# Optimization experiments

Measured on AMD Instinct MI355X. Metric: run time of the kernel, lower is better.

Reference implementation:

```python
import jax, jax.numpy as jnp
import numpy as np

B, S, H = 32, 256, 128
K, C, DSUB, O = 8, 4096, 16, 6  # PQ subspaces, ncentroids=4096, subvector dim, bits/symbol


def setup_inputs() -> dict:
    key = jax.random.key(0)
    ks = jax.random.split(key, 8)
    return {
        "z": jax.random.normal(ks[0], (B, S, 3), jnp.float32),
        "W1": jax.random.normal(ks[1], (3, H), jnp.float32) * 0.3,
        "b1": jax.random.normal(ks[2], (H,), jnp.float32) * 0.1,
        "W2": jax.random.normal(ks[3], (H, H), jnp.float32) * 0.1,
        "b2": jax.random.normal(ks[4], (H,), jnp.float32) * 0.1,
        "centroids": jax.random.normal(ks[5], (K, C, DSUB), jnp.float32),
        "W3": jax.random.normal(ks[6], (H, O), jnp.float32) * 0.1,
        "b3": jax.random.normal(ks[7], (O,), jnp.float32) * 0.1,
    }


def reference(z, W1, b1, W2, b2, centroids, W3, b3):
    # Small demapper MLP (layers 1-2, exact dense math)
    h1 = jax.nn.relu(z @ W1 + b1)            # [B,S,H]
    h2 = jax.nn.relu(h1 @ W2 + b2)           # [B,S,H] == layer3in
    N = B * S
    x = h2.reshape(N, K, DSUB)               # split rows into K PQ subvectors
    # Encode: nearest centroid per subspace (||x-c||^2 argmin; ||x||^2 is constant per row)
    dots = jnp.einsum("nkd,kcd->nkc", x, centroids)      # [N,K,C]
    c_norm = jnp.sum(centroids * centroids, axis=-1)      # [K,C]
    codes = jnp.argmin(c_norm[None, :, :] - 2.0 * dots, axis=-1)  # [N,K] int
    # LUT: precomputed centroid @ W3 per subspace
    W3r = W3.reshape(K, DSUB, O)
    lut = jnp.einsum("kcd,kdo->kco", centroids, W3r)      # [K,C,O]
    # Approximate matmul: sum of LUT entries selected by codes
    approx = jnp.sum(lut[jnp.arange(K)[None, :], codes], axis=1)  # [N,O]
    llr = (approx + b3).reshape(B, S * O)                 # [B, n]
    return llr
```

## Files before the change

kernel.cpp:

```cpp
#include <hip/hip_runtime.h>
#include <stdint.h>

#define NROWS 8192
#define HDIM  128
#define KSUB  8
#define NC    4096
#define DSUB  16
#define OUTD  6

#define FB_TAU 4e-3f
#define DOTSCALE (-2.0f / 4096.0f)

typedef _Float16 f16x8 __attribute__((ext_vector_type(8)));
typedef float    f32x4 __attribute__((ext_vector_type(4)));

#define XK_OFF 0u
#define CN_OFF 4194304u
#define B1_OFF 4325376u
#define B2_OFF 6422528u
#define CO_OFF 8519680u
#define MG_OFF 8781824u

__global__ __launch_bounds__(256) void bprep_kernel(
    const float* __restrict__ ce, f16x8* __restrict__ B1, f16x8* __restrict__ B2)
{
    const int e = blockIdx.x * 256 + threadIdx.x;
    const int k    = e >> 14;
    const int tile = (e >> 6) & 255;
    const int lane = e & 63;
    const int col  = lane & 15;
    const int quad = lane >> 4;
    const int dims = (quad & 1) * 8;
    const int part = quad >> 1;
    const int n = tile * 16 + col;
    const float* cp = &ce[((size_t)k * NC + n) * DSUB + dims];
    f16x8 hi, lo;
    #pragma unroll
    for (int j = 0; j < 8; ++j) {
        const float s = cp[j] * 16.0f;
        const _Float16 h = (_Float16)s;
        hi[j] = h;
        lo[j] = (_Float16)(s - (float)h);
    }
    B1[e] = part ? lo : hi;
    B2[e] = part ? hi : lo;
}

__global__ __launch_bounds__(256) void mlp_kernel(
    const float* __restrict__ z, const float* __restrict__ W1, const float* __restrict__ b1,
    const float* __restrict__ W2, const float* __restrict__ b2,
    const float* __restrict__ centroids,
    float* __restrict__ xk, float* __restrict__ cnorm)
{
    __shared__ float h1s[32 * HDIM];
    __shared__ float w2s[HDIM * HDIM];
    const int t = threadIdx.x;
    const int row0 = blockIdx.x * 32;

    if (blockIdx.x < (KSUB * NC) / 256) {
        const int g = blockIdx.x * 256 + t;
        const float4* cp = (const float4*)&centroids[(size_t)g * DSUB];
        float nn = 0.f;
        #pragma unroll
        for (int q = 0; q < 4; ++q) {
            const float4 v = cp[q];
            nn = fmaf(v.x, v.x, nn); nn = fmaf(v.y, v.y, nn);
            nn = fmaf(v.z, v.z, nn); nn = fmaf(v.w, v.w, nn);
        }
        cnorm[g] = nn;
    }

    {
        const float4* g4 = (const float4*)W2;
        float4* s4 = (float4*)w2s;
        #pragma unroll
        for (int q = 0; q < 16; ++q) s4[t + q * 256] = g4[t + q * 256];
    }

    #pragma unroll
    for (int e = 0; e < 16; ++e) {
        const int idx = e * 256 + t;
        const int r = idx >> 7, j = idx & 127;
        const int n = row0 + r;
        float acc = b1[j];
        acc = fmaf(z[n * 3 + 0], W1[0 * HDIM + j], acc);
        acc = fmaf(z[n * 3 + 1], W1[1 * HDIM + j], acc);
        acc = fmaf(z[n * 3 + 2], W1[2 * HDIM + j], acc);
        h1s[idx] = fmaxf(acc, 0.f);
    }
    __syncthreads();

    const int c4 = (t & 31) * 4;
    const int r4 = (t >> 5) * 4;
    float acc[4][4];
    #pragma unroll
    for (int a = 0; a < 4; ++a)
        #pragma unroll
        for (int b = 0; b < 4; ++b) acc[a][b] = 0.f;

    for (int k4 = 0; k4 < HDIM; k4 += 4) {
        float hh[4][4], ww[4][4];
        #pragma unroll
        for (int q = 0; q < 4; ++q) {
            const float4 v = *(const float4*)&h1s[(r4 + q) * HDIM + k4];
            hh[q][0] = v.x; hh[q][1] = v.y; hh[q][2] = v.z; hh[q][3] = v.w;
        }
        #pragma unroll
        for (int p = 0; p < 4; ++p) {
            const float4 v = *(const float4*)&w2s[(k4 + p) * HDIM + c4];
            ww[p][0] = v.x; ww[p][1] = v.y; ww[p][2] = v.z; ww[p][3] = v.w;
        }
        #pragma unroll
        for (int q = 0; q < 4; ++q)
            #pragma unroll
            for (int p = 0; p < 4; ++p) {
                acc[q][0] = fmaf(hh[q][p], ww[p][0], acc[q][0]);
                acc[q][1] = fmaf(hh[q][p], ww[p][1], acc[q][1]);
                acc[q][2] = fmaf(hh[q][p], ww[p][2], acc[q][2]);
                acc[q][3] = fmaf(hh[q][p], ww[p][3], acc[q][3]);
            }
    }

    const float4 bb = *(const float4*)&b2[c4];
    const int kk = c4 >> 4;
    const int dd = c4 & 15;
    #pragma unroll
    for (int q = 0; q < 4; ++q) {
        float4 o;
        o.x = fmaxf(acc[q][0] + bb.x, 0.f);
        o.y = fmaxf(acc[q][1] + bb.y, 0.f);
        o.z = fmaxf(acc[q][2] + bb.z, 0.f);
        o.w = fmaxf(acc[q][3] + bb.w, 0.f);
        *(float4*)&xk[((size_t)kk * NROWS + (row0 + r4 + q)) * DSUB + dd] = o;
    }
}

__global__ __launch_bounds__(256) void argmin_kernel(
    const float* __restrict__ xk, const f16x8* __restrict__ B1,
    const f16x8* __restrict__ B2, const float* __restrict__ cnorm,
    int* __restrict__ codes, float* __restrict__ margin)
{
    const int t = threadIdx.x;
    const int lane = t & 63;
    const int wid  = t >> 6;
    const int bx = blockIdx.x;
    const int k  = bx >> 6;
    const int rb = (bx & 63) * 4 + wid;
    const int col  = lane & 15;
    const int quad = lane >> 4;
    const int dims = (quad & 1) * 8;
    const int part = quad >> 1;

    f16x8 A[2];
    #pragma unroll
    for (int g = 0; g < 2; ++g) {
        const int row = rb * 32 + g * 16 + col;
        const float* xp = &xk[((size_t)k * NROWS + row) * DSUB + dims];
        f16x8 hi, lo;
        #pragma unroll
        for (int j = 0; j < 8; ++j) {
            const float s = xp[j] * 256.0f;
            const _Float16 h = (_Float16)s;
            hi[j] = h;
            lo[j] = (_Float16)(s - (float)h);
        }
        A[g] = part ? lo : hi;
    }

    float m1[2][4], m2[2][4];
    int   idx[2][4];
    #pragma unroll
    for (int g = 0; g < 2; ++g)
        #pragma unroll
        for (int j = 0; j < 4; ++j) { m1[g][j] = 1e30f; m2[g][j] = 1e30f; idx[g][j] = 0; }

    const f16x8* b1p = &B1[((size_t)k * 256) * 64 + lane];
    const f16x8* b2p = &B2[((size_t)k * 256) * 64 + lane];
    const float* cnp = &cnorm[k * NC + col];

    #pragma unroll 2
    for (int tt = 0; tt < 256; ++tt) {
        const f16x8 b1 = b1p[tt * 64];
        const f16x8 b2 = b2p[tt * 64];
        const float nrm = cnp[tt * 16];
        f32x4 acc0 = {0.f, 0.f, 0.f, 0.f};
        f32x4 acc1 = {0.f, 0.f, 0.f, 0.f};
        acc0 = __builtin_amdgcn_mfma_f32_16x16x32_f16(A[0], b1, acc0, 0, 0, 0);
        acc0 = __builtin_amdgcn_mfma_f32_16x16x32_f16(A[0], b2, acc0, 0, 0, 0);
        acc1 = __builtin_amdgcn_mfma_f32_16x16x32_f16(A[1], b1, acc1, 0, 0, 0);
        acc1 = __builtin_amdgcn_mfma_f32_16x16x32_f16(A[1], b2, acc1, 0, 0, 0);
        const int c = tt * 16 + col;
        #pragma unroll
        for (int j = 0; j < 4; ++j) {
            {
                const float s = fmaf(acc0[j], DOTSCALE, nrm);
                const bool lt = s < m1[0][j];
                m2[0][j] = fminf(m2[0][j], fmaxf(m1[0][j], s));
                idx[0][j] = lt ? c : idx[0][j];
                m1[0][j] = fminf(s, m1[0][j]);
            }
            {
                const float s = fmaf(acc1[j], DOTSCALE, nrm);
                const bool lt = s < m1[1][j];
                m2[1][j] = fminf(m2[1][j], fmaxf(m1[1][j], s));
                idx[1][j] = lt ? c : idx[1][j];
                m1[1][j] = fminf(s, m1[1][j]);
            }
        }
    }

    #pragma unroll
    for (int off = 1; off < 16; off <<= 1) {
        #pragma unroll
        for (int g = 0; g < 2; ++g)
            #pragma unroll
            for (int j = 0; j < 4; ++j) {
                const float om1 = __shfl_xor(m1[g][j], off, 64);
                const float om2 = __shfl_xor(m2[g][j], off, 64);
                const int  oidx = __shfl_xor(idx[g][j], off, 64);
                const bool better = (om1 < m1[g][j]) ||
                                    (om1 == m1[g][j] && oidx < idx[g][j]);
                m2[g][j] = fminf(fminf(m2[g][j], om2), fmaxf(m1[g][j], om1));
                m1[g][j] = better ? om1 : m1[g][j];
                idx[g][j] = better ? oidx : idx[g][j];
            }
    }

    if (col == 0) {
        #pragma unroll
        for (int g = 0; g < 2; ++g)
            #pragma unroll
            for (int j = 0; j < 4; ++j) {
                const int row = rb * 32 + g * 16 + quad * 4 + j;
                codes[row * KSUB + k] = idx[g][j];
                margin[row * KSUB + k] = m2[g][j] - m1[g][j];
            }
    }
}

__global__ __launch_bounds__(256) void fallback_kernel(
    const float* __restrict__ xk, const float* __restrict__ ce,
    const float* __restrict__ cnorm, const float* __restrict__ margin,
    int* __restrict__ codes)
{
    const int wg = blockIdx.x * 4 + (threadIdx.x >> 6);
    const int lane = threadIdx.x & 63;
    if (margin[wg] >= FB_TAU) return;
    const int row = wg >> 3, k = wg & 7;

    float xr[DSUB];
    {
        const float* xp = &xk[((size_t)k * NROWS + row) * DSUB];
        #pragma unroll
        for (int q = 0; q < DSUB; q += 4) {
            const float4 v = *(const float4*)&xp[q];
            xr[q + 0] = -2.f * v.x; xr[q + 1] = -2.f * v.y;
            xr[q + 2] = -2.f * v.z; xr[q + 3] = -2.f * v.w;
        }
    }
    float m1 = 1e30f; int mi = NC;
    for (int c = lane; c < NC; c += 64) {
        const float* cp = &ce[((size_t)k * NC + c) * DSUB];
        float s = cnorm[k * NC + c];
        #pragma unroll
        for (int d = 0; d < DSUB; ++d) s = fmaf(xr[d], cp[d], s);
        if (s < m1) { m1 = s; mi = c; }
    }
    #pragma unroll
    for (int off = 1; off < 64; off <<= 1) {
        const float om1 = __shfl_xor(m1, off, 64);
        const int  omi = __shfl_xor(mi, off, 64);
        const bool better = (om1 < m1) || (om1 == m1 && omi < mi);
        m1 = better ? om1 : m1;
        mi = better ? omi : mi;
    }
    if (lane == 0) codes[wg] = mi;
}

__global__ __launch_bounds__(256) void out_kernel(
    const float* __restrict__ centroids, const float* __restrict__ W3,
    const float* __restrict__ b3, const int* __restrict__ codes,
    float* __restrict__ out)
{
    const int gid = blockIdx.x * 256 + threadIdx.x;
    const int n = gid / OUTD;
    const int o = gid - n * OUTD;
    float acc = b3[o];
    #pragma unroll
    for (int k = 0; k < KSUB; ++k) {
        const int code = codes[n * KSUB + k];
        const float* cp = &centroids[((size_t)k * NC + code) * DSUB];
        const float* wp = &W3[(k * DSUB) * OUTD + o];
        #pragma unroll
        for (int d = 0; d < DSUB; ++d)
            acc = fmaf(cp[d], wp[d * OUTD], acc);
    }
    out[gid] = acc;
}

extern "C" void kernel_launch(void* const* d_in, const int* in_sizes, int n_in,
                              void* d_out, int out_size, void* d_ws, size_t ws_size,
                              hipStream_t stream)
{
    const float* z  = (const float*)d_in[0];
    const float* W1 = (const float*)d_in[1];
    const float* b1 = (const float*)d_in[2];
    const float* W2 = (const float*)d_in[3];
    const float* b2 = (const float*)d_in[4];
    const float* ce = (const float*)d_in[5];
    const float* W3 = (const float*)d_in[6];
    const float* b3 = (const float*)d_in[7];

    char* ws = (char*)d_ws;
    float* xk     = (float*)(ws + XK_OFF);
    float* cnorm  = (float*)(ws + CN_OFF);
    f16x8* B1     = (f16x8*)(ws + B1_OFF);
    f16x8* B2     = (f16x8*)(ws + B2_OFF);
    int*   codes  = (int*)  (ws + CO_OFF);
    float* margin = (float*)(ws + MG_OFF);

    hipLaunchKernelGGL(bprep_kernel, dim3(512), dim3(256), 0, stream, ce, B1, B2);
    hipLaunchKernelGGL(mlp_kernel, dim3(NROWS / 32), dim3(256), 0, stream,
                       z, W1, b1, W2, b2, ce, xk, cnorm);
    hipLaunchKernelGGL(argmin_kernel, dim3(512), dim3(256), 0, stream,
                       xk, B1, B2, cnorm, codes, margin);
    hipLaunchKernelGGL(fallback_kernel, dim3(NROWS * KSUB / 4), dim3(256), 0, stream,
                       xk, ce, cnorm, margin, codes);
    hipLaunchKernelGGL(out_kernel, dim3((NROWS * OUTD) / 256), dim3(256), 0, stream,
                       ce, W3, b3, codes, (float*)d_out);
}
```

Before: 208.6 us.

## Split argmin centroid range across two blocks and merge partial minima in fallback

The argmin kernel now splits the 4096 centroids into two halves along grid z, doubling the block count. Each half writes a packed orderable (score, index) key plus its second-best score, and the fallback kernel merges the two halves before its margin test. The kernel also drops the separate B2 buffer by reading B1 with lane^32, software-prefetches the next tile, uses independent MFMAs instead of chained accumulation, and uses fmed3 for the second-min update. In exchange it adds workspace traffic and an extra merge step, and codes now aliases the B1 region.

Result: faster. 194.7 us (-6.6%).

```diff
diff --git a/kernel.cpp b/kernel.cpp
--- a/kernel.cpp
+++ b/kernel.cpp
@@ -17,12 +17,12 @@
 #define XK_OFF 0u
 #define CN_OFF 4194304u
 #define B1_OFF 4325376u
-#define B2_OFF 6422528u
-#define CO_OFF 8519680u
-#define MG_OFF 8781824u
+#define PK_OFF 6422528u
+#define M2_OFF 7471104u
+#define CO_OFF B1_OFF
 
 __global__ __launch_bounds__(256) void bprep_kernel(
-    const float* __restrict__ ce, f16x8* __restrict__ B1, f16x8* __restrict__ B2)
+    const float* __restrict__ ce, f16x8* __restrict__ B1)
 {
     const int e = blockIdx.x * 256 + threadIdx.x;
     const int k    = e >> 14;
@@ -43,7 +43,6 @@
         lo[j] = (_Float16)(s - (float)h);
     }
     B1[e] = part ? lo : hi;
-    B2[e] = part ? hi : lo;
 }
 
 __global__ __launch_bounds__(256) void mlp_kernel(
@@ -135,21 +134,22 @@
     }
 }
 
-__global__ __launch_bounds__(256) void argmin_kernel(
+__global__ __launch_bounds__(256, 4) void argmin_kernel(
     const float* __restrict__ xk, const f16x8* __restrict__ B1,
-    const f16x8* __restrict__ B2, const float* __restrict__ cnorm,
-    int* __restrict__ codes, float* __restrict__ margin)
+    const float* __restrict__ cnorm,
+    unsigned long long* __restrict__ pk, float* __restrict__ m2s)
 {
     const int t = threadIdx.x;
     const int lane = t & 63;
     const int wid  = t >> 6;
-    const int bx = blockIdx.x;
-    const int k  = bx >> 6;
-    const int rb = (bx & 63) * 4 + wid;
+    const int k  = blockIdx.y;
+    const int cz = blockIdx.z;
+    const int rb = blockIdx.x * 4 + wid;
     const int col  = lane & 15;
     const int quad = lane >> 4;
     const int dims = (quad & 1) * 8;
     const int part = quad >> 1;
+    const int ct0 = cz * 128;
 
     f16x8 A[2];
     #pragma unroll
@@ -174,35 +174,40 @@
         #pragma unroll
         for (int j = 0; j < 4; ++j) { m1[g][j] = 1e30f; m2[g][j] = 1e30f; idx[g][j] = 0; }
 
-    const f16x8* b1p = &B1[((size_t)k * 256) * 64 + lane];
-    const f16x8* b2p = &B2[((size_t)k * 256) * 64 + lane];
-    const float* cnp = &cnorm[k * NC + col];
-
-    #pragma unroll 2
-    for (int tt = 0; tt < 256; ++tt) {
-        const f16x8 b1 = b1p[tt * 64];
-        const f16x8 b2 = b2p[tt * 64];
-        const float nrm = cnp[tt * 16];
-        f32x4 acc0 = {0.f, 0.f, 0.f, 0.f};
-        f32x4 acc1 = {0.f, 0.f, 0.f, 0.f};
-        acc0 = __builtin_amdgcn_mfma_f32_16x16x32_f16(A[0], b1, acc0, 0, 0, 0);
-        acc0 = __builtin_amdgcn_mfma_f32_16x16x32_f16(A[0], b2, acc0, 0, 0, 0);
-        acc1 = __builtin_amdgcn_mfma_f32_16x16x32_f16(A[1], b1, acc1, 0, 0, 0);
-        acc1 = __builtin_amdgcn_mfma_f32_16x16x32_f16(A[1], b2, acc1, 0, 0, 0);
-        const int c = tt * 16 + col;
+    const f16x8* bp = &B1[((size_t)k * 256 + ct0) * 64];
+    const float* cnp = &cnorm[k * NC + ct0 * 16 + col];
+    const int l2 = lane ^ 32;
+
+    f16x8 cb1 = bp[lane], cb2 = bp[l2];
+    float cnv = cnp[0];
+
+    for (int tt = 0; tt < 128; ++tt) {
+        const f16x8 b1 = cb1, b2 = cb2;
+        const float nrm = cnv;
+        if (tt + 1 < 128) {
+            cb1 = bp[(tt + 1) * 64 + lane];
+            cb2 = bp[(tt + 1) * 64 + l2];
+            cnv = cnp[(tt + 1) * 16];
+        }
+        f32x4 z4 = {0.f, 0.f, 0.f, 0.f};
+        f32x4 a0a = __builtin_amdgcn_mfma_f32_16x16x32_f16(A[0], b1, z4, 0, 0, 0);
+        f32x4 a0b = __builtin_amdgcn_mfma_f32_16x16x32_f16(A[0], b2, z4, 0, 0, 0);
+        f32x4 a1a = __builtin_amdgcn_mfma_f32_16x16x32_f16(A[1], b1, z4, 0, 0, 0);
+        f32x4 a1b = __builtin_amdgcn_mfma_f32_16x16x32_f16(A[1], b2, z4, 0, 0, 0);
+        const int c = (ct0 + tt) * 16 + col;
         #pragma unroll
         for (int j = 0; j < 4; ++j) {
             {
-                const float s = fmaf(acc0[j], DOTSCALE, nrm);
+                const float s = fmaf(a0a[j] + a0b[j], DOTSCALE, nrm);
                 const bool lt = s < m1[0][j];
-                m2[0][j] = fminf(m2[0][j], fmaxf(m1[0][j], s));
+                m2[0][j] = __builtin_amdgcn_fmed3f(s, m1[0][j], m2[0][j]);
                 idx[0][j] = lt ? c : idx[0][j];
                 m1[0][j] = fminf(s, m1[0][j]);
             }
             {
-                const float s = fmaf(acc1[j], DOTSCALE, nrm);
+                const float s = fmaf(a1a[j] + a1b[j], DOTSCALE, nrm);
                 const bool lt = s < m1[1][j];
-                m2[1][j] = fminf(m2[1][j], fmaxf(m1[1][j], s));
+                m2[1][j] = __builtin_amdgcn_fmed3f(s, m1[1][j], m2[1][j]);
                 idx[1][j] = lt ? c : idx[1][j];
                 m1[1][j] = fminf(s, m1[1][j]);
             }
@@ -232,22 +237,38 @@
             #pragma unroll
             for (int j = 0; j < 4; ++j) {
                 const int row = rb * 32 + g * 16 + quad * 4 + j;
-                codes[row * KSUB + k] = idx[g][j];
-                margin[row * KSUB + k] = m2[g][j] - m1[g][j];
+                unsigned u = __float_as_uint(m1[g][j]);
+                u = (u & 0x80000000u) ? ~u : (u | 0x80000000u);
+                pk [((size_t)cz * NROWS + row) * KSUB + k] =
+                    ((unsigned long long)u << 32) | (unsigned)idx[g][j];
+                m2s[((size_t)cz * NROWS + row) * KSUB + k] = m2[g][j];
             }
     }
 }
 
 __global__ __launch_bounds__(256) void fallback_kernel(
     const float* __restrict__ xk, const float* __restrict__ ce,
-    const float* __restrict__ cnorm, const float* __restrict__ margin,
-    int* __restrict__ codes)
+    const float* __restrict__ cnorm, const unsigned long long* __restrict__ pk,
+    const float* __restrict__ m2s, int* __restrict__ codes)
 {
     const int wg = blockIdx.x * 4 + (threadIdx.x >> 6);
     const int lane = threadIdx.x & 63;
-    if (margin[wg] >= FB_TAU) return;
+
+    const unsigned long long a = pk[wg];
+    const unsigned long long b = pk[(size_t)NROWS * KSUB + wg];
+    const unsigned long long w = a < b ? a : b;
+    const unsigned long long l = a < b ? b : a;
+    const unsigned uw = (unsigned)(w >> 32), ul = (unsigned)(l >> 32);
+    const float m1  = __uint_as_float((uw & 0x80000000u) ? (uw ^ 0x80000000u) : ~uw);
+    const float m1l = __uint_as_float((ul & 0x80000000u) ? (ul ^ 0x80000000u) : ~ul);
+    const float m2 = fminf(fminf(m2s[wg], m2s[(size_t)NROWS * KSUB + wg]), m1l);
+
+    if (m2 - m1 >= FB_TAU) {
+        if (lane == 0) codes[wg] = (int)(w & 0xFFFFFFFFull);
+        return;
+    }
+
     const int row = wg >> 3, k = wg & 7;
-
     float xr[DSUB];
     {
         const float* xp = &xk[((size_t)k * NROWS + row) * DSUB];
@@ -258,23 +279,23 @@
             xr[q + 2] = -2.f * v.z; xr[q + 3] = -2.f * v.w;
         }
     }
-    float m1 = 1e30f; int mi = NC;
+    float bm = 1e30f; int bi = NC;
     for (int c = lane; c < NC; c += 64) {
         const float* cp = &ce[((size_t)k * NC + c) * DSUB];
         float s = cnorm[k * NC + c];
         #pragma unroll
         for (int d = 0; d < DSUB; ++d) s = fmaf(xr[d], cp[d], s);
-        if (s < m1) { m1 = s; mi = c; }
+        if (s < bm) { bm = s; bi = c; }
     }
     #pragma unroll
     for (int off = 1; off < 64; off <<= 1) {
-        const float om1 = __shfl_xor(m1, off, 64);
-        const int  omi = __shfl_xor(mi, off, 64);
-        const bool better = (om1 < m1) || (om1 == m1 && omi < mi);
-        m1 = better ? om1 : m1;
-        mi = better ? omi : mi;
-    }
-    if (lane == 0) codes[wg] = mi;
+        const float om = __shfl_xor(bm, off, 64);
+        const int  oi = __shfl_xor(bi, off, 64);
+        const bool better = (om < bm) || (om == bm && oi < bi);
+        bm = better ? om : bm;
+        bi = better ? oi : bi;
+    }
+    if (lane == 0) codes[wg] = bi;
 }
 
 __global__ __launch_bounds__(256) void out_kernel(
@@ -315,17 +336,17 @@
     float* xk     = (float*)(ws + XK_OFF);
     float* cnorm  = (float*)(ws + CN_OFF);
     f16x8* B1     = (f16x8*)(ws + B1_OFF);
-    f16x8* B2     = (f16x8*)(ws + B2_OFF);
+    unsigned long long* pk = (unsigned long long*)(ws + PK_OFF);
+    float* m2s    = (float*)(ws + M2_OFF);
     int*   codes  = (int*)  (ws + CO_OFF);
-    float* margin = (float*)(ws + MG_OFF);
-
-    hipLaunchKernelGGL(bprep_kernel, dim3(512), dim3(256), 0, stream, ce, B1, B2);
+
+    hipLaunchKernelGGL(bprep_kernel, dim3(512), dim3(256), 0, stream, ce, B1);
     hipLaunchKernelGGL(mlp_kernel, dim3(NROWS / 32), dim3(256), 0, stream,
                        z, W1, b1, W2, b2, ce, xk, cnorm);
-    hipLaunchKernelGGL(argmin_kernel, dim3(512), dim3(256), 0, stream,
-                       xk, B1, B2, cnorm, codes, margin);
+    hipLaunchKernelGGL(argmin_kernel, dim3(64, 8, 2), dim3(256), 0, stream,
+                       xk, B1, cnorm, pk, m2s);
     hipLaunchKernelGGL(fallback_kernel, dim3(NROWS * KSUB / 4), dim3(256), 0, stream,
-                       xk, ce, cnorm, margin, codes);
+                       xk, ce, cnorm, pk, m2s, codes);
     hipLaunchKernelGGL(out_kernel, dim3((NROWS * OUTD) / 256), dim3(256), 0, stream,
                        ce, W3, b3, codes, (float*)d_out);
 }
```
